# Kernel optimization log

Measured on AMD Instinct MI355X. Metric: run time of the kernel, lower is better.

The kernel has to match this reference:

```python
import jax, jax.numpy as jnp
import numpy as np

B, H, S, D = 4, 16, 4096, 64

def setup_inputs() -> dict:
    key = jax.random.key(0)
    kq, kk, kv, km = jax.random.split(key, 4)
    Q = jax.random.normal(kq, (B, H, S, D), dtype=jnp.float32)
    K = jax.random.normal(kk, (B, H, S, D), dtype=jnp.float32)
    V = jax.random.normal(kv, (B, H, S, D), dtype=jnp.float32)
    mask = jax.random.randint(km, (B, S), 0, 2, dtype=jnp.int32)
    return {"Q": Q, "K": K, "V": V, "mask": mask}

def reference(Q, K, V, mask):
    Q = jax.nn.relu(Q)
    K = jax.nn.relu(K)
    # zero out masked-out key positions: mask [B,S] -> [B,1,S,1]
    m = mask.astype(bool)[:, None, :, None]
    K = jnp.where(m, K, jnp.zeros((), K.dtype))
    # attn_inter = K^T V : [B,H,D,D]
    attn_inter = jnp.einsum('bhsd,bhse->bhde', K, V)
    # attn_weights = Q @ attn_inter : [B,H,S,D]
    attn_weights = jnp.einsum('bhsd,bhde->bhse', Q, attn_inter)
    # norm = Q @ sum_s K : [B,H,S,1]
    k_sum = K.sum(axis=2)  # [B,H,D]
    norm = jnp.einsum('bhsd,bhd->bhs', Q, k_sum)[..., None]
    return attn_weights / norm
```

## Files before the change

kernel.cpp:

```cpp
#include <hip/hip_runtime.h>

#define SDIM 4096
#define DDIM 64
#define HN   16
#define BH   64
#define NC   16

typedef __attribute__((ext_vector_type(8))) short short8;
typedef __attribute__((ext_vector_type(4))) float f32x4;

static __device__ __forceinline__ unsigned short f2bf(float f) {
    unsigned u = __float_as_uint(f);
    return (unsigned short)((u + 0x7FFFu + ((u >> 16) & 1u)) >> 16);
}

__global__ __launch_bounds__(256) void k1_kv(
    const float* __restrict__ K, const float* __restrict__ V,
    const int* __restrict__ mask,
    float* __restrict__ KVp, float* __restrict__ ksump)
{
    __shared__ float red[4 * 2176];
    const int tid  = threadIdx.x;
    const int w    = tid >> 6;
    const int l    = tid & 63;
    const int r16  = l & 15;
    const int quad = l >> 4;
    const int bh = blockIdx.x / NC;
    const int ch = blockIdx.x % NC;
    const int b  = bh / HN;
    const long base = (long)bh * SDIM * DDIM;
    const int s0 = ch * (SDIM / NC) + w * 64;

    const int* mrow = mask + b * SDIM + s0 + quad * 8;
    float mv[2][8];
#pragma unroll
    for (int kh = 0; kh < 2; ++kh)
#pragma unroll
        for (int j = 0; j < 8; ++j)
            mv[kh][j] = mrow[kh * 32 + j] ? 1.f : 0.f;

    const float* kp = K + base + (long)(s0 + quad * 8) * DDIM + r16;
    const float* vp = V + base + (long)(s0 + quad * 8) * DDIM + r16;
    short8 afrag[2][4], bfrag[2][4];
#pragma unroll
    for (int kh = 0; kh < 2; ++kh)
#pragma unroll
        for (int dt = 0; dt < 4; ++dt) {
            short8 ta, tb;
#pragma unroll
            for (int j = 0; j < 8; ++j) {
                float kv = kp[(kh * 32 + j) * DDIM + dt * 16];
                kv = fmaxf(kv, 0.f) * mv[kh][j];
                ta[j] = (short)f2bf(kv);
                tb[j] = (short)f2bf(vp[(kh * 32 + j) * DDIM + dt * 16]);
            }
            afrag[kh][dt] = ta;
            bfrag[kh][dt] = tb;
        }

    f32x4 acc[4][4];
#pragma unroll
    for (int i = 0; i < 4; ++i)
#pragma unroll
        for (int j = 0; j < 4; ++j) acc[i][j] = (f32x4){0.f, 0.f, 0.f, 0.f};
    f32x4 kacc[4];
#pragma unroll
    for (int i = 0; i < 4; ++i) kacc[i] = (f32x4){0.f, 0.f, 0.f, 0.f};
    short8 ones;
#pragma unroll
    for (int j = 0; j < 8; ++j) ones[j] = (short)0x3F80;

#pragma unroll
    for (int kh = 0; kh < 2; ++kh) {
#pragma unroll
        for (int dt = 0; dt < 4; ++dt) {
#pragma unroll
            for (int et = 0; et < 4; ++et)
                acc[dt][et] = __builtin_amdgcn_mfma_f32_16x16x32_bf16(
                    afrag[kh][dt], bfrag[kh][et], acc[dt][et], 0, 0, 0);
            kacc[dt] = __builtin_amdgcn_mfma_f32_16x16x32_bf16(
                afrag[kh][dt], ones, kacc[dt], 0, 0, 0);
        }
    }

    float* outp = KVp + ((long)bh * NC + ch) * 4096;
#pragma unroll
    for (int h = 0; h < 2; ++h) {
        __syncthreads();
#pragma unroll
        for (int dt = 0; dt < 2; ++dt)
#pragma unroll
            for (int et = 0; et < 4; ++et)
#pragma unroll
                for (int r = 0; r < 4; ++r)
                    red[w * 2176 + (dt * 16 + quad * 4 + r) * 68 +
                        et * 16 + r16] = acc[h * 2 + dt][et][r];
        __syncthreads();
#pragma unroll
        for (int i = 0; i < 8; ++i) {
            const int idx = i * 256 + tid;
            const int d = idx >> 6, e = idx & 63;
            outp[h * 2048 + idx] =
                red[d * 68 + e] + red[2176 + d * 68 + e] +
                red[4352 + d * 68 + e] + red[6528 + d * 68 + e];
        }
    }
    __syncthreads();
    if (r16 == 0) {
#pragma unroll
        for (int dt = 0; dt < 4; ++dt)
#pragma unroll
            for (int r = 0; r < 4; ++r)
                red[w * 64 + dt * 16 + quad * 4 + r] = kacc[dt][r];
    }
    __syncthreads();
    if (tid < 64) {
        ksump[((long)bh * NC + ch) * 64 + tid] =
            red[tid] + red[64 + tid] + red[128 + tid] + red[192 + tid];
    }
}

__global__ __launch_bounds__(256) void k2_reduce(
    const float* __restrict__ KVp, const float* __restrict__ ksump,
    float* __restrict__ KV, float* __restrict__ ksum)
{
    const int bh = blockIdx.x >> 2;
    const int qt = blockIdx.x & 3;
    const int tid = threadIdx.x;
#pragma unroll
    for (int i = 0; i < 4; ++i) {
        const int idx = qt * 1024 + i * 256 + tid;
        float v = 0.f;
#pragma unroll
        for (int c = 0; c < NC; ++c) v += KVp[((long)bh * NC + c) * 4096 + idx];
        KV[(long)bh * 4096 + idx] = v;
    }
    if (qt == 0 && tid < 64) {
        float v = 0.f;
#pragma unroll
        for (int c = 0; c < NC; ++c) v += ksump[((long)bh * NC + c) * 64 + tid];
        ksum[bh * 64 + tid] = v;
    }
}

__global__ __launch_bounds__(256, 4) void k3_out(
    const float* __restrict__ Q, const float* __restrict__ KVm,
    const float* __restrict__ ksum, float* __restrict__ out)
{
    __shared__ float cbuf[4][16 * 68];
    const int tid  = threadIdx.x;
    const int w    = tid >> 6;
    const int l    = tid & 63;
    const int r16  = l & 15;
    const int quad = l >> 4;
    const int bh    = blockIdx.x >> 4;
    const int strip = blockIdx.x & 15;

    const float* kvp = KVm + (long)bh * 4096;
    short8 bfrag[2][4];
#pragma unroll
    for (int kh = 0; kh < 2; ++kh)
#pragma unroll
        for (int n = 0; n < 4; ++n) {
            short8 tmp;
#pragma unroll
            for (int j = 0; j < 8; ++j)
                tmp[j] = (short)f2bf(kvp[(kh * 32 + quad * 8 + j) * 64 + n * 16 + r16]);
            bfrag[kh][n] = tmp;
        }
    float ksv[16];
#pragma unroll
    for (int j = 0; j < 8; ++j) {
        ksv[j]     = ksum[bh * 64 + quad * 8 + j];
        ksv[j + 8] = ksum[bh * 64 + 32 + quad * 8 + j];
    }

    const int rowbase = strip * 256 + w * 64;
    const float* qptr = Q + ((long)bh * SDIM + rowbase + r16) * DDIM + quad * 8;
    float* obase = out + ((long)bh * SDIM + rowbase) * DDIM;
    float* cw = &cbuf[w][0];

    f32x4 a0 = *(const f32x4*)(qptr);
    f32x4 a1 = *(const f32x4*)(qptr + 4);
    f32x4 a2 = *(const f32x4*)(qptr + 32);
    f32x4 a3 = *(const f32x4*)(qptr + 36);

    for (int t = 0; t < 4; ++t) {
        f32x4 b0 = a0, b1 = a1, b2 = a2, b3 = a3;
        if (t < 3) {
            const float* qn = qptr + (t + 1) * 16 * DDIM;
            b0 = *(const f32x4*)(qn);
            b1 = *(const f32x4*)(qn + 4);
            b2 = *(const f32x4*)(qn + 32);
            b3 = *(const f32x4*)(qn + 36);
        }
#pragma unroll
        for (int j = 0; j < 4; ++j) {
            a0[j] = fmaxf(a0[j], 0.f); a1[j] = fmaxf(a1[j], 0.f);
            a2[j] = fmaxf(a2[j], 0.f); a3[j] = fmaxf(a3[j], 0.f);
        }
        float p = 0.f;
#pragma unroll
        for (int j = 0; j < 4; ++j) {
            p = fmaf(a0[j], ksv[j],      p);
            p = fmaf(a1[j], ksv[4 + j],  p);
            p = fmaf(a2[j], ksv[8 + j],  p);
            p = fmaf(a3[j], ksv[12 + j], p);
        }
        p += __shfl_xor(p, 16);
        p += __shfl_xor(p, 32);
        const float inv = __builtin_amdgcn_rcpf(p);

        short8 af0, af1;
#pragma unroll
        for (int j = 0; j < 4; ++j) {
            af0[j]     = (short)f2bf(a0[j]);
            af0[4 + j] = (short)f2bf(a1[j]);
            af1[j]     = (short)f2bf(a2[j]);
            af1[4 + j] = (short)f2bf(a3[j]);
        }

        f32x4 acc[4];
#pragma unroll
        for (int n = 0; n < 4; ++n) {
            acc[n] = (f32x4){0.f, 0.f, 0.f, 0.f};
            acc[n] = __builtin_amdgcn_mfma_f32_16x16x32_bf16(af0, bfrag[0][n], acc[n], 0, 0, 0);
            acc[n] = __builtin_amdgcn_mfma_f32_16x16x32_bf16(af1, bfrag[1][n], acc[n], 0, 0, 0);
        }

        float invr[4];
#pragma unroll
        for (int r = 0; r < 4; ++r) invr[r] = __shfl(inv, quad * 4 + r);

#pragma unroll
        for (int n = 0; n < 4; ++n)
#pragma unroll
            for (int r = 0; r < 4; ++r)
                cw[(quad * 4 + r) * 68 + n * 16 + r16] = acc[n][r] * invr[r];

        float* ot = obase + (t * 16) * DDIM;
#pragma unroll
        for (int i = 0; i < 4; ++i) {
            f32x4 v = *(const f32x4*)(cw + (i * 4 + quad) * 68 + r16 * 4);
            *(f32x4*)(ot + (i * 4 + quad) * DDIM + r16 * 4) = v;
        }
        a0 = b0; a1 = b1; a2 = b2; a3 = b3;
    }
}

extern "C" void kernel_launch(void* const* d_in, const int* in_sizes, int n_in,
                              void* d_out, int out_size, void* d_ws, size_t ws_size,
                              hipStream_t stream)
{
    const float* Q    = (const float*)d_in[0];
    const float* K    = (const float*)d_in[1];
    const float* V    = (const float*)d_in[2];
    const int*   mask = (const int*)d_in[3];
    float* out = (float*)d_out;

    float* KVp   = out;
    float* ksump = KVp + (long)BH * NC * 4096;
    float* KV    = (float*)d_ws;
    float* ksum  = KV + (long)BH * 4096;

    hipLaunchKernelGGL(k1_kv, dim3(BH * NC), dim3(256), 0, stream,
                       K, V, mask, KVp, ksump);
    hipLaunchKernelGGL(k2_reduce, dim3(BH * 4), dim3(256), 0, stream,
                       KVp, ksump, KV, ksum);
    hipLaunchKernelGGL(k3_out, dim3(BH * 16), dim3(256), 0, stream,
                       Q, KV, ksum, out);
}
```

Baseline: 59.40 us.

## Stage K/V tiles through LDS and split output columns across waves in KV kernel

The first kernel now loads K and V with coalesced float4 reads into padded shared-memory tiles, processing four 64-row sub-chunks per block with register prefetch of the next sub-chunk. Each wave computes a distinct 16-column slice of the 64x64 K^T V output over all rows, so the cross-wave shared-memory reduction is removed and results are written directly. Previously each lane issued strided scalar global loads. The change adds LDS round-trips and bank traffic, extra barriers per sub-chunk, and a launch-bounds occupancy hint.

```diff
diff --git a/kernel.cpp b/kernel.cpp
--- a/kernel.cpp
+++ b/kernel.cpp
@@ -14,109 +14,106 @@
     return (unsigned short)((u + 0x7FFFu + ((u >> 16) & 1u)) >> 16);
 }
 
-__global__ __launch_bounds__(256) void k1_kv(
+__global__ __launch_bounds__(256, 4) void k1_kv(
     const float* __restrict__ K, const float* __restrict__ V,
     const int* __restrict__ mask,
     float* __restrict__ KVp, float* __restrict__ ksump)
 {
-    __shared__ float red[4 * 2176];
+    __shared__ float Ks[64 * 65];
+    __shared__ float Vs[64 * 65];
     const int tid  = threadIdx.x;
     const int w    = tid >> 6;
     const int l    = tid & 63;
     const int r16  = l & 15;
     const int quad = l >> 4;
-    const int bh = blockIdx.x / NC;
-    const int ch = blockIdx.x % NC;
-    const int b  = bh / HN;
+    const int bh = blockIdx.x >> 4;
+    const int ch = blockIdx.x & 15;
+    const int b  = bh >> 4;
     const long base = (long)bh * SDIM * DDIM;
-    const int s0 = ch * (SDIM / NC) + w * 64;
-
-    const int* mrow = mask + b * SDIM + s0 + quad * 8;
-    float mv[2][8];
-#pragma unroll
-    for (int kh = 0; kh < 2; ++kh)
-#pragma unroll
-        for (int j = 0; j < 8; ++j)
-            mv[kh][j] = mrow[kh * 32 + j] ? 1.f : 0.f;
-
-    const float* kp = K + base + (long)(s0 + quad * 8) * DDIM + r16;
-    const float* vp = V + base + (long)(s0 + quad * 8) * DDIM + r16;
-    short8 afrag[2][4], bfrag[2][4];
-#pragma unroll
-    for (int kh = 0; kh < 2; ++kh)
-#pragma unroll
-        for (int dt = 0; dt < 4; ++dt) {
-            short8 ta, tb;
-#pragma unroll
-            for (int j = 0; j < 8; ++j) {
-                float kv = kp[(kh * 32 + j) * DDIM + dt * 16];
-                kv = fmaxf(kv, 0.f) * mv[kh][j];
-                ta[j] = (short)f2bf(kv);
-                tb[j] = (short)f2bf(vp[(kh * 32 + j) * DDIM + dt * 16]);
+    const int s0 = ch * 256;
+
+    const int sr = tid >> 4;
+    const int sc = (tid & 15) << 2;
+
+    float4 kreg[4], vreg[4];
+    int    mreg[4];
+#pragma unroll
+    for (int i = 0; i < 4; ++i) {
+        const int r = sr + i * 16;
+        kreg[i] = *(const float4*)(K + base + (long)(s0 + r) * DDIM + sc);
+        vreg[i] = *(const float4*)(V + base + (long)(s0 + r) * DDIM + sc);
+        mreg[i] = mask[b * SDIM + s0 + r];
+    }
+
+    f32x4 acc[4];
+#pragma unroll
+    for (int i = 0; i < 4; ++i) acc[i] = (f32x4){0.f, 0.f, 0.f, 0.f};
+    f32x4 kacc = (f32x4){0.f, 0.f, 0.f, 0.f};
+    short8 ones;
+#pragma unroll
+    for (int j = 0; j < 8; ++j) ones[j] = (short)0x3F80;
+
+    for (int t = 0; t < 4; ++t) {
+        __syncthreads();
+#pragma unroll
+        for (int i = 0; i < 4; ++i) {
+            const float m = mreg[i] ? 1.f : 0.f;
+            float4 kq = kreg[i];
+            kq.x = fmaxf(kq.x, 0.f) * m;
+            kq.y = fmaxf(kq.y, 0.f) * m;
+            kq.z = fmaxf(kq.z, 0.f) * m;
+            kq.w = fmaxf(kq.w, 0.f) * m;
+            *(float4*)(Ks + (sr + i * 16) * 65 + sc) = kq;
+            *(float4*)(Vs + (sr + i * 16) * 65 + sc) = vreg[i];
+        }
+        __syncthreads();
+        if (t < 3) {
+            const int r0n = s0 + (t + 1) * 64;
+#pragma unroll
+            for (int i = 0; i < 4; ++i) {
+                const int r = sr + i * 16;
+                kreg[i] = *(const float4*)(K + base + (long)(r0n + r) * DDIM + sc);
+                vreg[i] = *(const float4*)(V + base + (long)(r0n + r) * DDIM + sc);
+                mreg[i] = mask[b * SDIM + r0n + r];
             }
-            afrag[kh][dt] = ta;
-            bfrag[kh][dt] = tb;
-        }
-
-    f32x4 acc[4][4];
-#pragma unroll
-    for (int i = 0; i < 4; ++i)
-#pragma unroll
-        for (int j = 0; j < 4; ++j) acc[i][j] = (f32x4){0.f, 0.f, 0.f, 0.f};
-    f32x4 kacc[4];
-#pragma unroll
-    for (int i = 0; i < 4; ++i) kacc[i] = (f32x4){0.f, 0.f, 0.f, 0.f};
-    short8 ones;
-#pragma unroll
-    for (int j = 0; j < 8; ++j) ones[j] = (short)0x3F80;
-
-#pragma unroll
-    for (int kh = 0; kh < 2; ++kh) {
-#pragma unroll
-        for (int dt = 0; dt < 4; ++dt) {
-#pragma unroll
-            for (int et = 0; et < 4; ++et)
-                acc[dt][et] = __builtin_amdgcn_mfma_f32_16x16x32_bf16(
-                    afrag[kh][dt], bfrag[kh][et], acc[dt][et], 0, 0, 0);
-            kacc[dt] = __builtin_amdgcn_mfma_f32_16x16x32_bf16(
-                afrag[kh][dt], ones, kacc[dt], 0, 0, 0);
+        }
+#pragma unroll
+        for (int kh = 0; kh < 2; ++kh) {
+            const int sb = kh * 32 + quad * 8;
+            short8 af[4];
+#pragma unroll
+            for (int dt = 0; dt < 4; ++dt) {
+                short8 ta;
+#pragma unroll
+                for (int j = 0; j < 8; ++j)
+                    ta[j] = (short)f2bf(Ks[(sb + j) * 65 + dt * 16 + r16]);
+                af[dt] = ta;
+            }
+            short8 bf;
+#pragma unroll
+            for (int j = 0; j < 8; ++j)
+                bf[j] = (short)f2bf(Vs[(sb + j) * 65 + w * 16 + r16]);
+#pragma unroll
+            for (int dt = 0; dt < 4; ++dt)
+                acc[dt] = __builtin_amdgcn_mfma_f32_16x16x32_bf16(
+                    af[dt], bf, acc[dt], 0, 0, 0);
+            kacc = __builtin_amdgcn_mfma_f32_16x16x32_bf16(
+                af[w], ones, kacc, 0, 0, 0);
         }
     }
 
     float* outp = KVp + ((long)bh * NC + ch) * 4096;
 #pragma unroll
-    for (int h = 0; h < 2; ++h) {
-        __syncthreads();
-#pragma unroll
-        for (int dt = 0; dt < 2; ++dt)
-#pragma unroll
-            for (int et = 0; et < 4; ++et)
-#pragma unroll
-                for (int r = 0; r < 4; ++r)
-                    red[w * 2176 + (dt * 16 + quad * 4 + r) * 68 +
-                        et * 16 + r16] = acc[h * 2 + dt][et][r];
-        __syncthreads();
-#pragma unroll
-        for (int i = 0; i < 8; ++i) {
-            const int idx = i * 256 + tid;
-            const int d = idx >> 6, e = idx & 63;
-            outp[h * 2048 + idx] =
-                red[d * 68 + e] + red[2176 + d * 68 + e] +
-                red[4352 + d * 68 + e] + red[6528 + d * 68 + e];
-        }
-    }
-    __syncthreads();
+    for (int dt = 0; dt < 4; ++dt)
+#pragma unroll
+        for (int r = 0; r < 4; ++r) {
+            const int d = dt * 16 + quad * 4 + r;
+            outp[d * 64 + w * 16 + r16] = acc[dt][r];
+        }
     if (r16 == 0) {
 #pragma unroll
-        for (int dt = 0; dt < 4; ++dt)
-#pragma unroll
-            for (int r = 0; r < 4; ++r)
-                red[w * 64 + dt * 16 + quad * 4 + r] = kacc[dt][r];
-    }
-    __syncthreads();
-    if (tid < 64) {
-        ksump[((long)bh * NC + ch) * 64 + tid] =
-            red[tid] + red[64 + tid] + red[128 + tid] + red[192 + tid];
+        for (int r = 0; r < 4; ++r)
+            ksump[((long)bh * NC + ch) * 64 + w * 16 + quad * 4 + r] = kacc[r];
     }
 }
 
```

Result: slower. 98.09 us (+65.1%).
